# Kernel tuning notes

Measured on AMD Instinct MI355X. Metric: run time of the kernel, lower is better.

The kernel has to match this reference:

```python
import jax, jax.numpy as jnp
from jax import lax
import numpy as np

I, H = 16, 32  # input_size, hidden_size
B, T = 8192, 512


def setup_inputs() -> dict:
    key = jax.random.key(0)
    ks = jax.random.split(key, 8)
    s_ih = 1.0 / np.sqrt(H)
    x = jax.random.normal(ks[0], (B, T, I), dtype=jnp.float32)
    # PyTorch LSTM params, gate order i,f,g,o along the 4H dim
    W_ih = jax.random.uniform(ks[1], (4 * H, I), minval=-s_ih, maxval=s_ih, dtype=jnp.float32)
    W_hh = jax.random.uniform(ks[2], (4 * H, H), minval=-s_ih, maxval=s_ih, dtype=jnp.float32)
    b_ih = jax.random.uniform(ks[3], (4 * H,), minval=-s_ih, maxval=s_ih, dtype=jnp.float32)
    b_hh = jax.random.uniform(ks[4], (4 * H,), minval=-s_ih, maxval=s_ih, dtype=jnp.float32)
    W_fc = jax.random.uniform(ks[5], (1, H), minval=-s_ih, maxval=s_ih, dtype=jnp.float32)
    b_fc = jax.random.uniform(ks[6], (1,), minval=-s_ih, maxval=s_ih, dtype=jnp.float32)
    return {"x": x, "W_ih": W_ih, "W_hh": W_hh, "b_ih": b_ih, "b_hh": b_hh,
            "W_fc": W_fc, "b_fc": b_fc}


def reference(x, W_ih, W_hh, b_ih, b_hh, W_fc, b_fc):
    # Precompute input contribution for all timesteps: [B, T, 4H]
    xg = jnp.einsum('bti,gi->btg', x, W_ih) + b_ih + b_hh

    def step(carry, g_t):  # g_t: [B, 4H]
        h, c = carry
        gates = g_t + h @ W_hh.T
        i, f, g, o = jnp.split(gates, 4, axis=-1)
        c = jax.nn.sigmoid(f) * c + jax.nn.sigmoid(i) * jnp.tanh(g)
        h = jax.nn.sigmoid(o) * jnp.tanh(c)
        return (h, c), None

    h0 = jnp.zeros((x.shape[0], H), dtype=x.dtype)
    (h_last, _), _ = lax.scan(step, (h0, h0), jnp.swapaxes(xg, 0, 1))
    # last_hidden -> dropout (eval mode: identity) -> fc -> squeeze
    out = h_last @ W_fc.T + b_fc  # [B, 1]
    return out.squeeze(-1)  # [B]
```

## Files before the change

kernel.cpp:

```cpp
#include <hip/hip_runtime.h>


typedef short short4v __attribute__((ext_vector_type(4)));
typedef __bf16 bf4 __attribute__((ext_vector_type(4)));
typedef float f4 __attribute__((ext_vector_type(4)));

constexpr int ISZ = 16, HSZ = 32, TT = 512, BB = 8192;
constexpr int LDS_STRIDE = 40;

#define MFMA16(a, b, c) __builtin_amdgcn_mfma_f32_16x16x16bf16_1k((a), (b), (c), 0, 0, 0)

__device__ __forceinline__ float fsig(float x) {
  return __builtin_amdgcn_rcpf(1.0f + __builtin_amdgcn_exp2f(-1.44269504f * x));
}

__device__ __forceinline__ void split4(f4 v, short4v& hi, short4v& lo) {
  bf4 b1, b2;
#pragma unroll
  for (int i = 0; i < 4; ++i) b1[i] = (__bf16)v[i];
#pragma unroll
  for (int i = 0; i < 4; ++i) b2[i] = (__bf16)(v[i] - (float)b1[i]);
  hi = __builtin_bit_cast(short4v, b1);
  lo = __builtin_bit_cast(short4v, b2);
}

__global__ __launch_bounds__(512, 4) void lstm_mfma(
    const float* __restrict__ x, const float* __restrict__ W_ih,
    const float* __restrict__ W_hh, const float* __restrict__ b_ih,
    const float* __restrict__ b_hh, const float* __restrict__ W_fc,
    const float* __restrict__ b_fc, float* __restrict__ out) {
  __shared__ __align__(16) __bf16 hlds[2][2][16][LDS_STRIDE];
  __shared__ __align__(16) float gbuf[4][16][HSZ + 1];

  const int tid = threadIdx.x;
  const int wv = tid >> 6;
  const int g = wv & 3;
  const int uh = wv >> 2;
  const int L = tid & 63;
  const int m = L & 15;
  const int q = L >> 4;
  const int row0 = blockIdx.x * 16;
  const int uw = uh * 16 + m;
  const int j = g * 32 + uw;

  const int eR = wv * 2 + (L >> 5);
  const int eu = L & 31;

  short4v whh1a, whh1b, whh2a, whh2b, wih1, wih2;
  f4 biasv;
  {
    f4 wa = *(const f4*)(W_hh + j * HSZ + q * 4);
    f4 wb = *(const f4*)(W_hh + j * HSZ + 16 + q * 4);
    split4(wa, whh1a, whh2a);
    split4(wb, whh1b, whh2b);
    f4 wi = *(const f4*)(W_ih + j * ISZ + q * 4);
    split4(wi, wih1, wih2);
    const float bb = b_ih[j] + b_hh[j];
    biasv = (f4){bb, bb, bb, bb};
  }

  for (int i = tid; i < 2 * 2 * 16 * LDS_STRIDE; i += 512)
    ((__bf16*)hlds)[i] = (__bf16)0.0f;
  __syncthreads();

  float cst = 0.0f;

  const float* xrow = x + (size_t)(row0 + m) * TT * ISZ + q * 4;
  f4 xc = *(const f4*)xrow;

  for (int t = 0; t < TT; ++t) {
    const int p = t & 1;
    const short4v h1a = *(const short4v*)&hlds[p][0][m][q * 4];
    const short4v h1b = *(const short4v*)&hlds[p][0][m][16 + q * 4];
    const short4v h2a = *(const short4v*)&hlds[p][1][m][q * 4];
    const short4v h2b = *(const short4v*)&hlds[p][1][m][16 + q * 4];

    const int tn = (t < TT - 1) ? t + 1 : t;
    const f4 xn = *(const f4*)(xrow + tn * ISZ);

    short4v x1, x2;
    split4(xc, x1, x2);

    f4 a = MFMA16(x1, wih1, biasv);
    a = MFMA16(x2, wih1, a);
    a = MFMA16(x1, wih2, a);
    a = MFMA16(h1a, whh1a, a);
    a = MFMA16(h1b, whh1b, a);
    a = MFMA16(h2a, whh1a, a);
    a = MFMA16(h2b, whh1b, a);
    a = MFMA16(h1a, whh2a, a);
    a = MFMA16(h1b, whh2b, a);
    xc = xn;

#pragma unroll
    for (int r = 0; r < 4; ++r) gbuf[g][q * 4 + r][uw] = a[r];
    __syncthreads();

    const float vi = gbuf[0][eR][eu];
    const float vf = gbuf[1][eR][eu];
    const float vg = gbuf[2][eR][eu];
    const float vo = gbuf[3][eR][eu];

    const float ig = fsig(vi);
    const float fg = fsig(vf);
    const float gv = 2.0f * fsig(2.0f * vg) - 1.0f;
    const float og = fsig(vo);
    float cc = fg * cst + ig * gv;
    cst = cc;
    const float th = 2.0f * fsig(2.0f * cc) - 1.0f;
    const float h = og * th;
    const __bf16 h1 = (__bf16)h;
    const __bf16 h2 = (__bf16)(h - (float)h1);
    hlds[p ^ 1][0][eR][eu] = h1;
    hlds[p ^ 1][1][eR][eu] = h2;
    __syncthreads();
  }

  if (tid < 16) {
    float s = b_fc[0];
#pragma unroll 8
    for (int uu = 0; uu < HSZ; ++uu) {
      const float h = (float)hlds[0][0][tid][uu] + (float)hlds[0][1][tid][uu];
      s += h * W_fc[uu];
    }
    out[row0 + tid] = s;
  }
}

extern "C" void kernel_launch(void* const* d_in, const int* in_sizes, int n_in,
                              void* d_out, int out_size, void* d_ws, size_t ws_size,
                              hipStream_t stream) {
  const float* x    = (const float*)d_in[0];
  const float* W_ih = (const float*)d_in[1];
  const float* W_hh = (const float*)d_in[2];
  const float* b_ih = (const float*)d_in[3];
  const float* b_hh = (const float*)d_in[4];
  const float* W_fc = (const float*)d_in[5];
  const float* b_fc = (const float*)d_in[6];
  float* out = (float*)d_out;

  dim3 grid(BB / 16);
  dim3 block(512);
  lstm_mfma<<<grid, block, 0, stream>>>(x, W_ih, W_hh, b_ih, b_hh, W_fc, b_fc, out);
}
```

Before: 683.6 us.

## Use 16x16x32 bf16 MFMA with concatenated hi/lo operands and LDS-staged x

Switches from the 16x16x16 bf16 MFMA to the wider 16x16x32 variant, packing the hi/lo split halves of h and x along the K dimension so the recurrent step needs 5 MFMAs instead of 9. The next x timestep is now loaded by 256 threads (one element each), split into bf16 hi/lo in the elementwise phase, and written to a double-buffered LDS tile, so no wave has to split x per step. This shortens the serial MFMA chain on the critical path of each timestep. The cost is extra LDS writes and a wider per-step x load pattern.

```diff
diff --git a/kernel.cpp b/kernel.cpp
--- a/kernel.cpp
+++ b/kernel.cpp
@@ -1,27 +1,26 @@
 #include <hip/hip_runtime.h>
 
 
-typedef short short4v __attribute__((ext_vector_type(4)));
-typedef __bf16 bf4 __attribute__((ext_vector_type(4)));
 typedef float f4 __attribute__((ext_vector_type(4)));
+typedef __bf16 bf8v __attribute__((ext_vector_type(8)));
 
 constexpr int ISZ = 16, HSZ = 32, TT = 512, BB = 8192;
-constexpr int LDS_STRIDE = 40;
+constexpr int HSTR = 72;
+constexpr int XSTR = 40;
 
-#define MFMA16(a, b, c) __builtin_amdgcn_mfma_f32_16x16x16bf16_1k((a), (b), (c), 0, 0, 0)
+#define MFMA32(a, b, c) __builtin_amdgcn_mfma_f32_16x16x32_bf16((a), (b), (c), 0, 0, 0)
 
 __device__ __forceinline__ float fsig(float x) {
   return __builtin_amdgcn_rcpf(1.0f + __builtin_amdgcn_exp2f(-1.44269504f * x));
 }
 
-__device__ __forceinline__ void split4(f4 v, short4v& hi, short4v& lo) {
-  bf4 b1, b2;
+__device__ __forceinline__ void split8(const float* v, bf8v& hi, bf8v& lo) {
 #pragma unroll
-  for (int i = 0; i < 4; ++i) b1[i] = (__bf16)v[i];
-#pragma unroll
-  for (int i = 0; i < 4; ++i) b2[i] = (__bf16)(v[i] - (float)b1[i]);
-  hi = __builtin_bit_cast(short4v, b1);
-  lo = __builtin_bit_cast(short4v, b2);
+  for (int i = 0; i < 8; ++i) {
+    const __bf16 h = (__bf16)v[i];
+    hi[i] = h;
+    lo[i] = (__bf16)(v[i] - (float)h);
+  }
 }
 
 __global__ __launch_bounds__(512, 4) void lstm_mfma(
@@ -29,7 +28,8 @@
     const float* __restrict__ W_hh, const float* __restrict__ b_ih,
     const float* __restrict__ b_hh, const float* __restrict__ W_fc,
     const float* __restrict__ b_fc, float* __restrict__ out) {
-  __shared__ __align__(16) __bf16 hlds[2][2][16][LDS_STRIDE];
+  __shared__ __align__(16) __bf16 hl[2][16][HSTR];
+  __shared__ __align__(16) __bf16 xs[2][16][XSTR];
   __shared__ __align__(16) float gbuf[4][16][HSZ + 1];
 
   const int tid = threadIdx.x;
@@ -46,51 +46,50 @@
   const int eR = wv * 2 + (L >> 5);
   const int eu = L & 31;
 
-  short4v whh1a, whh1b, whh2a, whh2b, wih1, wih2;
+  bf8v bih1, bih2, bhh1, bhh2;
   f4 biasv;
   {
-    f4 wa = *(const f4*)(W_hh + j * HSZ + q * 4);
-    f4 wb = *(const f4*)(W_hh + j * HSZ + 16 + q * 4);
-    split4(wa, whh1a, whh2a);
-    split4(wb, whh1b, whh2b);
-    f4 wi = *(const f4*)(W_ih + j * ISZ + q * 4);
-    split4(wi, wih1, wih2);
+    float wh[8];
+    *(f4*)&wh[0] = *(const f4*)(W_hh + j * HSZ + 8 * q);
+    *(f4*)&wh[4] = *(const f4*)(W_hh + j * HSZ + 8 * q + 4);
+    split8(wh, bhh1, bhh2);
+    float wi[8];
+    const int k8 = (q & 1) * 8;
+    *(f4*)&wi[0] = *(const f4*)(W_ih + j * ISZ + k8);
+    *(f4*)&wi[4] = *(const f4*)(W_ih + j * ISZ + k8 + 4);
+    split8(wi, bih1, bih2);
     const float bb = b_ih[j] + b_hh[j];
     biasv = (f4){bb, bb, bb, bb};
   }
 
-  for (int i = tid; i < 2 * 2 * 16 * LDS_STRIDE; i += 512)
-    ((__bf16*)hlds)[i] = (__bf16)0.0f;
+  for (int i = tid; i < 2 * 16 * HSTR; i += 512) ((__bf16*)hl)[i] = (__bf16)0.0f;
+  const int xr = tid >> 4, xi = tid & 15;
+  const float* xbase = x + (size_t)(row0 + xr) * TT * ISZ + xi;
+  if (tid < 256) {
+    const float v = xbase[0];
+    const __bf16 h = (__bf16)v;
+    xs[0][xr][xi] = h;
+    xs[0][xr][16 + xi] = (__bf16)(v - (float)h);
+  }
   __syncthreads();
 
   float cst = 0.0f;
 
-  const float* xrow = x + (size_t)(row0 + m) * TT * ISZ + q * 4;
-  f4 xc = *(const f4*)xrow;
-
   for (int t = 0; t < TT; ++t) {
     const int p = t & 1;
-    const short4v h1a = *(const short4v*)&hlds[p][0][m][q * 4];
-    const short4v h1b = *(const short4v*)&hlds[p][0][m][16 + q * 4];
-    const short4v h2a = *(const short4v*)&hlds[p][1][m][q * 4];
-    const short4v h2b = *(const short4v*)&hlds[p][1][m][16 + q * 4];
+    const bf8v ax  = *(const bf8v*)&xs[p][m][8 * q];
+    const bf8v ah1 = *(const bf8v*)&hl[p][m][8 * q];
+    const bf8v ah2 = *(const bf8v*)&hl[p][m][32 + 8 * q];
 
+    float xnext = 0.0f;
     const int tn = (t < TT - 1) ? t + 1 : t;
-    const f4 xn = *(const f4*)(xrow + tn * ISZ);
+    if (tid < 256) xnext = xbase[(size_t)tn * ISZ];
 
-    short4v x1, x2;
-    split4(xc, x1, x2);
-
-    f4 a = MFMA16(x1, wih1, biasv);
-    a = MFMA16(x2, wih1, a);
-    a = MFMA16(x1, wih2, a);
-    a = MFMA16(h1a, whh1a, a);
-    a = MFMA16(h1b, whh1b, a);
-    a = MFMA16(h2a, whh1a, a);
-    a = MFMA16(h2b, whh1b, a);
-    a = MFMA16(h1a, whh2a, a);
-    a = MFMA16(h1b, whh2b, a);
-    xc = xn;
+    f4 a = MFMA32(ax, bih1, biasv);
+    a = MFMA32(ax, bih2, a);
+    a = MFMA32(ah1, bhh1, a);
+    a = MFMA32(ah2, bhh1, a);
+    a = MFMA32(ah1, bhh2, a);
 
 #pragma unroll
     for (int r = 0; r < 4; ++r) gbuf[g][q * 4 + r][uw] = a[r];
@@ -105,14 +104,19 @@
     const float fg = fsig(vf);
     const float gv = 2.0f * fsig(2.0f * vg) - 1.0f;
     const float og = fsig(vo);
-    float cc = fg * cst + ig * gv;
+    const float cc = fg * cst + ig * gv;
     cst = cc;
     const float th = 2.0f * fsig(2.0f * cc) - 1.0f;
     const float h = og * th;
     const __bf16 h1 = (__bf16)h;
-    const __bf16 h2 = (__bf16)(h - (float)h1);
-    hlds[p ^ 1][0][eR][eu] = h1;
-    hlds[p ^ 1][1][eR][eu] = h2;
+    hl[p ^ 1][eR][eu] = h1;
+    hl[p ^ 1][eR][32 + eu] = (__bf16)(h - (float)h1);
+
+    if (tid < 256) {
+      const __bf16 xh = (__bf16)xnext;
+      xs[p ^ 1][xr][xi] = xh;
+      xs[p ^ 1][xr][16 + xi] = (__bf16)(xnext - (float)xh);
+    }
     __syncthreads();
   }
 
@@ -120,7 +124,7 @@
     float s = b_fc[0];
 #pragma unroll 8
     for (int uu = 0; uu < HSZ; ++uu) {
-      const float h = (float)hlds[0][0][tid][uu] + (float)hlds[0][1][tid][uu];
+      const float h = (float)hl[0][tid][uu] + (float)hl[0][tid][32 + uu];
       s += h * W_fc[uu];
     }
     out[row0 + tid] = s;
```

After: 629.4 us. 7.9% less time.
